# Optimization experiments

Measured on AMD Instinct MI355X. Metric: run time of the kernel, lower is better.

## Reference

```python
import jax, jax.numpy as jnp
import numpy as np

GROUP_SIZE = 128


def setup_inputs() -> dict:
    key = jax.random.key(0)
    k1, k2, k3, k4, k5 = jax.random.split(key, 5)
    N, I, O = 16, 4096, 11008
    Ng = I // GROUP_SIZE  # 32
    x = jax.random.normal(k1, (N, I), dtype=jnp.float16)
    # raw int8 bit patterns, represented as int32 in [0, 256) (== value after & 255)
    weight_q = jax.random.randint(k2, (O, I), 0, 256, dtype=jnp.int32)
    scale = (jax.random.uniform(k3, (O, Ng), dtype=jnp.float32) * 0.01 + 0.001).astype(jnp.float16)
    zero = (jax.random.uniform(k4, (O, Ng), dtype=jnp.float32) * 255.0).astype(jnp.float16)
    bias = (jax.random.normal(k5, (O,), dtype=jnp.float32) * 0.02).astype(jnp.float16)
    return {"x": x, "weight_q": weight_q, "scale": scale, "zero": zero, "bias": bias}


def reference(x, weight_q, scale, zero, bias):
    O, I = weight_q.shape
    G = GROUP_SIZE
    Ng = I // G  # I divisible by G here, so no padding branch
    # (weight_q.int16 & 255).uint8 -> fp16, group-wise dequant
    wq = (weight_q & 255).astype(jnp.float16).reshape(O, Ng, G)
    w_fp = (scale[:, :, None] * (wq - zero[:, :, None])).reshape(O, I)  # (O, I) fp16
    # F.linear(x, w_fp, bias)
    return jnp.dot(x, w_fp.T) + bias
```

## Files before the change

kernel.cpp:

```cpp
#include <hip/hip_runtime.h>
#include <hip/hip_fp16.h>


typedef _Float16 v8hf __attribute__((ext_vector_type(8)));
typedef float v4f __attribute__((ext_vector_type(4)));

#define O_DIM 11008
#define I_DIM 4096
#define NGROUP 32

__global__ __launch_bounds__(256) void init_out(const float* __restrict__ bias,
                                                float* __restrict__ out) {
    int t = blockIdx.x * 256 + threadIdx.x;
    int o = t % O_DIM;
    out[t] = bias[o];
}

__global__ __launch_bounds__(256) void qgemm(const float* __restrict__ x,
                                             const int* __restrict__ wq,
                                             const float* __restrict__ scale,
                                             const float* __restrict__ zero,
                                             float* __restrict__ out) {
    const int b   = blockIdx.x;
    const int ot  = b >> 2;
    const int kc  = b & 3;
    const int tid = threadIdx.x;
    const int w   = tid >> 6;
    const int l   = tid & 63;
    const int col = l & 15;
    const int kb  = l >> 4;
    const int o   = ot * 16 + col;

    const int* __restrict__ wrow = wq + (size_t)o * I_DIM;

    v4f acc = {0.f, 0.f, 0.f, 0.f};

#pragma unroll
    for (int gi = 0; gi < 2; ++gi) {
        const int g = kc * 8 + w * 2 + gi;
        const float s   = scale[o * NGROUP + g];
        const float z   = zero [o * NGROUP + g];
        const float nzs = -z * s;
#pragma unroll
        for (int ks = 0; ks < 4; ++ks) {
            const int i0 = g * 128 + ks * 32;
            const int* wp = wrow + i0 + kb * 8;
            const int4 q0 = *(const int4*)(wp);
            const int4 q1 = *(const int4*)(wp + 4);
            const float* xp = x + (size_t)col * I_DIM + i0 + kb * 8;
            const float4 x0 = *(const float4*)(xp);
            const float4 x1 = *(const float4*)(xp + 4);
            v8hf a;
            a[0] = (_Float16)x0.x; a[1] = (_Float16)x0.y;
            a[2] = (_Float16)x0.z; a[3] = (_Float16)x0.w;
            a[4] = (_Float16)x1.x; a[5] = (_Float16)x1.y;
            a[6] = (_Float16)x1.z; a[7] = (_Float16)x1.w;
            v8hf bf;
            bf[0] = (_Float16)((float)(q0.x & 255) * s + nzs);
            bf[1] = (_Float16)((float)(q0.y & 255) * s + nzs);
            bf[2] = (_Float16)((float)(q0.z & 255) * s + nzs);
            bf[3] = (_Float16)((float)(q0.w & 255) * s + nzs);
            bf[4] = (_Float16)((float)(q1.x & 255) * s + nzs);
            bf[5] = (_Float16)((float)(q1.y & 255) * s + nzs);
            bf[6] = (_Float16)((float)(q1.z & 255) * s + nzs);
            bf[7] = (_Float16)((float)(q1.w & 255) * s + nzs);
            acc = __builtin_amdgcn_mfma_f32_16x16x32_f16(a, bf, acc, 0, 0, 0);
        }
    }

    float* op = out + (size_t)(kb * 4) * O_DIM + o;
#pragma unroll
    for (int r = 0; r < 4; ++r) {
        atomicAdd(op + (size_t)r * O_DIM, acc[r]);
    }
}

extern "C" void kernel_launch(void* const* d_in, const int* in_sizes, int n_in,
                              void* d_out, int out_size, void* d_ws, size_t ws_size,
                              hipStream_t stream) {
    const float* x   = (const float*)d_in[0];
    const int*   wqp = (const int*)  d_in[1];
    const float* sc  = (const float*)d_in[2];
    const float* zp  = (const float*)d_in[3];
    const float* bp  = (const float*)d_in[4];
    float* out = (float*)d_out;

    init_out<<<688, 256, 0, stream>>>(bp, out);
    qgemm<<<2752, 256, 0, stream>>>(x, wqp, sc, zp, out);
}
```

Before: 55.18 us.

## Replace split-K atomics with in-block LDS reduction and fuse bias init

```diff
diff --git a/kernel.cpp b/kernel.cpp
--- a/kernel.cpp
+++ b/kernel.cpp
@@ -9,21 +9,15 @@
 #define I_DIM 4096
 #define NGROUP 32
 
-__global__ __launch_bounds__(256) void init_out(const float* __restrict__ bias,
-                                                float* __restrict__ out) {
-    int t = blockIdx.x * 256 + threadIdx.x;
-    int o = t % O_DIM;
-    out[t] = bias[o];
-}
-
 __global__ __launch_bounds__(256) void qgemm(const float* __restrict__ x,
                                              const int* __restrict__ wq,
                                              const float* __restrict__ scale,
                                              const float* __restrict__ zero,
+                                             const float* __restrict__ bias,
                                              float* __restrict__ out) {
-    const int b   = blockIdx.x;
-    const int ot  = b >> 2;
-    const int kc  = b & 3;
+    __shared__ float red[4][256];
+
+    const int ot  = blockIdx.x;
     const int tid = threadIdx.x;
     const int w   = tid >> 6;
     const int l   = tid & 63;
@@ -31,25 +25,24 @@
     const int kb  = l >> 4;
     const int o   = ot * 16 + col;
 
-    const int* __restrict__ wrow = wq + (size_t)o * I_DIM;
+    const int*   __restrict__ wrow = wq + (size_t)o * I_DIM;
+    const float* __restrict__ xrow = x  + (size_t)col * I_DIM;
 
     v4f acc = {0.f, 0.f, 0.f, 0.f};
 
-#pragma unroll
-    for (int gi = 0; gi < 2; ++gi) {
-        const int g = kc * 8 + w * 2 + gi;
+#pragma unroll 2
+    for (int gi = 0; gi < 8; ++gi) {
+        const int g = w * 8 + gi;
         const float s   = scale[o * NGROUP + g];
         const float z   = zero [o * NGROUP + g];
         const float nzs = -z * s;
 #pragma unroll
         for (int ks = 0; ks < 4; ++ks) {
-            const int i0 = g * 128 + ks * 32;
-            const int* wp = wrow + i0 + kb * 8;
-            const int4 q0 = *(const int4*)(wp);
-            const int4 q1 = *(const int4*)(wp + 4);
-            const float* xp = x + (size_t)col * I_DIM + i0 + kb * 8;
-            const float4 x0 = *(const float4*)(xp);
-            const float4 x1 = *(const float4*)(xp + 4);
+            const int i0 = g * 128 + ks * 32 + kb * 8;
+            const int4   q0 = *(const int4*)  (wrow + i0);
+            const int4   q1 = *(const int4*)  (wrow + i0 + 4);
+            const float4 x0 = *(const float4*)(xrow + i0);
+            const float4 x1 = *(const float4*)(xrow + i0 + 4);
             v8hf a;
             a[0] = (_Float16)x0.x; a[1] = (_Float16)x0.y;
             a[2] = (_Float16)x0.z; a[3] = (_Float16)x0.w;
@@ -68,11 +61,16 @@
         }
     }
 
-    float* op = out + (size_t)(kb * 4) * O_DIM + o;
-#pragma unroll
-    for (int r = 0; r < 4; ++r) {
-        atomicAdd(op + (size_t)r * O_DIM, acc[r]);
-    }
+    *(v4f*)&red[w][l * 4] = acc;
+    __syncthreads();
+
+    const int t   = tid;
+    const float sum = red[0][t] + red[1][t] + red[2][t] + red[3][t];
+    const int l2  = t >> 2;
+    const int r   = t & 3;
+    const int row = (l2 >> 4) * 4 + r;
+    const int oc  = ot * 16 + (l2 & 15);
+    out[(size_t)row * O_DIM + oc] = sum + bias[oc];
 }
 
 extern "C" void kernel_launch(void* const* d_in, const int* in_sizes, int n_in,
@@ -85,6 +83,5 @@
     const float* bp  = (const float*)d_in[4];
     float* out = (float*)d_out;
 
-    init_out<<<688, 256, 0, stream>>>(bp, out);
-    qgemm<<<2752, 256, 0, stream>>>(x, wqp, sc, zp, out);
+    qgemm<<<688, 256, 0, stream>>>(x, wqp, sc, zp, bp, out);
 }
```

New measurement: 51.19 us. 1.08x faster.
